# Kernel optimization log

Hardware: AMD Instinct MI355X
Metric: run time of the kernel (lower is better)

## Reference

```python
import jax, jax.numpy as jnp
import numpy as np

B = 48        # graphs
NPG = 64      # nodes per graph
N = B * NPG   # 3072 total nodes
E = B * NPG * NPG  # 196608 fully-connected intra-graph edges
EMB = 8       # ldm latent size
HID = 128     # hidden_size
OUT = 128     # out_size
NL = 3        # n_layers


def setup_inputs() -> dict:
    key = jax.random.key(0)
    ks = jax.random.split(key, 20)
    H = jax.random.normal(ks[0], (N, EMB), jnp.float32)
    Z = jax.random.normal(ks[1], (N, 1, 3), jnp.float32)
    beta = jax.random.uniform(ks[2], (N,), jnp.float32)
    batch_ids = jnp.repeat(jnp.arange(B, dtype=jnp.int32), NPG)
    # variadic_meshgrid: fully-connected edges within each graph
    base = np.arange(B, dtype=np.int32)[:, None, None] * NPG
    r = np.broadcast_to(np.arange(NPG, dtype=np.int32)[:, None], (NPG, NPG))
    row = (base + r[None]).reshape(-1)
    col = (base + r.T[None]).reshape(-1)
    edges = jnp.asarray(np.stack([row, col], axis=0), jnp.int32)

    def lin(k, fan_in, fan_out):
        return jax.random.normal(k, (fan_in, fan_out), jnp.float32) / jnp.sqrt(jnp.float32(fan_in))

    params = {
        'W_emb': lin(ks[3], EMB + 3, HID), 'b_emb': jnp.zeros((HID,), jnp.float32),
        'We1': jnp.stack([lin(jax.random.fold_in(ks[4], l), 2 * HID + 1, HID) for l in range(NL)]),
        'be1': jnp.zeros((NL, HID), jnp.float32),
        'We2': jnp.stack([lin(jax.random.fold_in(ks[5], l), HID, HID) for l in range(NL)]),
        'be2': jnp.zeros((NL, HID), jnp.float32),
        'Wn1': jnp.stack([lin(jax.random.fold_in(ks[6], l), 2 * HID, HID) for l in range(NL)]),
        'bn1': jnp.zeros((NL, HID), jnp.float32),
        'Wn2': jnp.stack([lin(jax.random.fold_in(ks[7], l), HID, HID) for l in range(NL)]),
        'bn2': jnp.zeros((NL, HID), jnp.float32),
        'Wo1': lin(ks[8], HID, HID), 'bo1': jnp.zeros((HID,), jnp.float32),
        'Wo2': lin(ks[9], HID, OUT), 'bo2': jnp.zeros((OUT,), jnp.float32),
    }
    return dict(H=H, Z=Z, beta=beta, batch_ids=batch_ids, edges=edges, **params)


def reference(H, Z, beta, batch_ids, edges, W_emb, b_emb, We1, be1, We2, be2,
              Wn1, bn1, Wn2, bn2, Wo1, bo1, Wo2, bo2):
    # t_embed = [beta, sin(beta), cos(beta)] per node, concatenated to latent H
    t_embed = jnp.stack([beta, jnp.sin(beta), jnp.cos(beta)], axis=-1)  # [N,3]
    h = jnp.concatenate([H, t_embed], axis=-1) @ W_emb + b_emb          # [N,HID]

    row, col = edges[0], edges[1]
    # squared pairwise distance over (channel, xyz)
    d2 = jnp.sum((Z[row] - Z[col]) ** 2, axis=(1, 2))[:, None]          # [E,1]

    # EGNN-style message passing (stand-in for EPT/AMEGNN encoder)
    for l in range(NL):
        m = jax.nn.silu(jnp.concatenate([h[row], h[col], d2], axis=-1) @ We1[l] + be1[l])
        m = jax.nn.silu(m @ We2[l] + be2[l])                            # [E,HID]
        agg = jax.ops.segment_sum(m, row, num_segments=N)               # [N,HID]
        h = h + jax.nn.silu(jnp.concatenate([h, agg], axis=-1) @ Wn1[l] + bn1[l]) @ Wn2[l] + bn2[l]

    # std_conserve_scatter_sum readout: segment-sum / sqrt(count)
    counts = jax.ops.segment_sum(jnp.ones((N,), h.dtype), batch_ids, num_segments=B)
    g = jax.ops.segment_sum(h, batch_ids, num_segments=B) / jnp.sqrt(counts)[:, None]  # [B,HID]

    # linear_out: SiLU -> Linear -> SiLU -> Linear
    out = jax.nn.silu(g) @ Wo1 + bo1
    out = jax.nn.silu(out) @ Wo2 + bo2                                   # [B,OUT]
    return out
```

## Files before the change

kernel.cpp:

```cpp
#include <hip/hip_runtime.h>

#define NGRAPH 48
#define ALPHA 1.44269504088896340736f
#define LN2   0.69314718055994530942f

typedef __bf16 bf16x8 __attribute__((ext_vector_type(8)));
typedef float  f32x16 __attribute__((ext_vector_type(16)));

__device__ __forceinline__ f32x16 MFMA(bf16x8 a, bf16x8 b, f32x16 c) {
  return __builtin_amdgcn_mfma_f32_32x32x16_bf16(a, b, c, 0, 0, 0);
}

__device__ __forceinline__ float fsilu(float x) {
  return x * __builtin_amdgcn_rcpf(1.0f + __expf(-x));
}
__device__ __forceinline__ float ssilu(float s) {
  return s * __builtin_amdgcn_rcpf(1.0f + __builtin_amdgcn_exp2f(-s));
}

__global__ __launch_bounds__(256) void prep_kernel(
    const float* We1, const float* We2, const float* Wn1, const float* Wn2,
    __bf16* We1T, __bf16* We2T, __bf16* Wn1T, __bf16* Wn2T, float* wv) {
  int i = blockIdx.x * 256 + threadIdx.x;
  const int S0 = 3 * 256 * 128;
  const int S1 = 3 * 128 * 128;
  const int S2 = 3 * 128 * 256;
  const int S3 = 3 * 128 * 128;
  const int S4 = 3 * 128;
  if (i < S0) {
    int l = i / (256 * 128); int r = i % (256 * 128); int n = r / 128; int k = r % 128;
    float v = (n < 128) ? We1[(l * 257 + k) * 128 + n]
                        : We1[(l * 257 + 128 + k) * 128 + (n - 128)];
    We1T[i] = (__bf16)v; return;
  }
  i -= S0;
  if (i < S1) {
    int l = i / (128 * 128); int r = i % (128 * 128); int n = r / 128, k = r % 128;
    We2T[i] = (__bf16)We2[(l * 128 + k) * 128 + n]; return;
  }
  i -= S1;
  if (i < S2) {
    int l = i / (128 * 256); int r = i % (128 * 256); int n = r / 256, k = r % 256;
    float sc = (k >= 128) ? LN2 : 1.0f;
    Wn1T[i] = (__bf16)(Wn1[(l * 256 + k) * 128 + n] * sc); return;
  }
  i -= S2;
  if (i < S3) {
    int l = i / (128 * 128); int r = i % (128 * 128); int n = r / 128, k = r % 128;
    Wn2T[i] = (__bf16)Wn2[(l * 128 + k) * 128 + n]; return;
  }
  i -= S3;
  if (i < S4) {
    int l = i / 128, k = i % 128;
    wv[i] = ALPHA * We1[(l * 257 + 256) * 128 + k];
  }
}

__device__ __forceinline__ void pq_stage(const float* hn,
    const __bf16* We1Tl, const float* be1l, float* Pp, __bf16* Qb, int r0, int t) {
  int lane = t & 63, wid = t >> 6;
  int l31 = lane & 31, q = lane >> 5;
  bf16x8 af[8];
#pragma unroll
  for (int kk = 0; kk < 8; ++kk) {
    int k0 = kk * 16 + q * 8;
    const float* ap = &hn[l31 * 132 + k0];
#pragma unroll
    for (int j = 0; j < 8; ++j) af[kk][j] = (__bf16)ap[j];
  }
#pragma unroll
  for (int half = 0; half < 2; ++half) {
    int nt = wid * 2 + half;
    f32x16 acc;
#pragma unroll
    for (int r = 0; r < 16; ++r) acc[r] = 0.f;
#pragma unroll
    for (int kk = 0; kk < 8; ++kk) {
      int k0 = kk * 16 + q * 8;
      bf16x8 b = *(const bf16x8*)&We1Tl[(nt * 32 + l31) * 128 + k0];
      acc = MFMA(af[kk], b, acc);
    }
    int col = nt * 32 + l31;
    if (col < 128) {
      float bb = be1l[col];
#pragma unroll
      for (int reg = 0; reg < 16; ++reg) {
        int rr = (reg & 3) + 8 * (reg >> 2) + 4 * q;
        Pp[(r0 + rr) * 128 + col] = (acc[reg] + bb) * ALPHA;
      }
    } else {
      int c2 = col - 128;
#pragma unroll
      for (int reg = 0; reg < 16; ++reg) {
        int rr = (reg & 3) + 8 * (reg >> 2) + 4 * q;
        Qb[(r0 + rr) * 128 + c2] = (__bf16)(acc[reg] * ALPHA);
      }
    }
  }
}

__global__ __launch_bounds__(256) void embed_kernel(
    const float* H, const float* beta, const float* W_emb, const float* b_emb,
    const __bf16* We1T0, const float* be1_0,
    float* h, float* Pp, __bf16* Qb) {
  __shared__ float Hs[256];
  __shared__ float bet[32], sb[32], cb[32];
  __shared__ float hns[32 * 132];
  int t = threadIdx.x; int r0 = blockIdx.x * 32;
  Hs[t] = H[r0 * 8 + t];
  if (t < 32) {
    float b = beta[r0 + t];
    bet[t] = b; sb[t] = sinf(b); cb[t] = cosf(b);
  }
  __syncthreads();
#pragma unroll
  for (int i = 0; i < 16; ++i) {
    int c = t + 256 * i;
    int row = c >> 7, n = c & 127;
    float acc = b_emb[n];
#pragma unroll
    for (int k = 0; k < 8; ++k) acc += Hs[row * 8 + k] * W_emb[k * 128 + n];
    acc += bet[row] * W_emb[8 * 128 + n] + sb[row] * W_emb[9 * 128 + n]
         + cb[row] * W_emb[10 * 128 + n];
    hns[row * 132 + n] = acc;
    h[(r0 + row) * 128 + n] = acc;
  }
  __syncthreads();
  pq_stage(hns, We1T0, be1_0, Pp, Qb, r0, t);
}

__global__ __launch_bounds__(512)
__attribute__((amdgpu_waves_per_eu(4, 4)))
void edge_kernel(
    const float* __restrict__ Ppin, const __bf16* __restrict__ Qbin,
    const float* __restrict__ Z, const float* __restrict__ wvg,
    const __bf16* __restrict__ We2Tl, const float* __restrict__ be2l,
    float* __restrict__ agg) {
  __shared__ __bf16 Qs[64 * 132];
  __shared__ __bf16 WeTs[128 * 132];
  __shared__ float  Ps[4 * 132];
  __shared__ float  aggp[8][132];
  __shared__ float  Zs[192];
  __shared__ float  wvs[128];
  __shared__ float  be2s[128];
  int t = threadIdx.x;
  int g = blockIdx.x >> 4, atile = blockIdx.x & 15;
  int a0 = atile * 4, gn0 = g * 64;
#pragma unroll
  for (int i = 0; i < 2; ++i) {
    int c = t + 512 * i; int row = c >> 4, c8 = (c & 15) * 8;
    *(uint4*)&Qs[row * 132 + c8] = *(const uint4*)&Qbin[(gn0 + row) * 128 + c8];
  }
#pragma unroll
  for (int i = 0; i < 4; ++i) {
    int c = t + 512 * i; int row = c >> 4, c8 = (c & 15) * 8;
    *(uint4*)&WeTs[row * 132 + c8] = *(const uint4*)&We2Tl[row * 128 + c8];
  }
  if (t < 128) {
    int row = t >> 5, c4 = (t & 31) * 4;
    *(float4*)&Ps[row * 132 + c4] = *(const float4*)&Ppin[(gn0 + a0 + row) * 128 + c4];
    wvs[t] = wvg[t];
    be2s[t] = ALPHA * be2l[t];
  }
  if (t < 192) Zs[t] = Z[gn0 * 3 + t];
  __syncthreads();

  int lane = t & 63, wid = t >> 6, l31 = lane & 31, q = lane >> 5;
  int a_loc = wid >> 1, bhalf = wid & 1;
  int a_g = a0 + a_loc;
  int b = bhalf * 32 + l31;

  float zax = Zs[a_g * 3], zay = Zs[a_g * 3 + 1], zaz = Zs[a_g * 3 + 2];
  float dx = zax - Zs[b * 3], dy = zay - Zs[b * 3 + 1], dz = zaz - Zs[b * 3 + 2];
  float d2 = dx * dx + dy * dy + dz * dz;

  bf16x8 af[8];
#pragma unroll
  for (int kk = 0; kk < 8; ++kk) {
    int k0 = kk * 16 + q * 8;
    float4 pv0 = *(const float4*)&Ps[a_loc * 132 + k0];
    float4 pv1 = *(const float4*)&Ps[a_loc * 132 + k0 + 4];
    float4 wv0 = *(const float4*)&wvs[k0];
    float4 wv1 = *(const float4*)&wvs[k0 + 4];
    bf16x8 qv = *(const bf16x8*)&Qs[b * 132 + k0];
#pragma unroll
    for (int j = 0; j < 4; ++j) {
      af[kk][j]     = (__bf16)ssilu(fmaf(d2, wv0[j], pv0[j]) + (float)qv[j]);
      af[kk][j + 4] = (__bf16)ssilu(fmaf(d2, wv1[j], pv1[j]) + (float)qv[j + 4]);
    }
  }
  float smv[4];
#pragma unroll
  for (int np = 0; np < 2; ++np) {
    f32x16 accA, accB;
#pragma unroll
    for (int r = 0; r < 16; ++r) { accA[r] = 0.f; accB[r] = 0.f; }
#pragma unroll
    for (int kk = 0; kk < 8; ++kk) {
      int ko = kk * 16 + q * 8;
      accA = MFMA(af[kk], *(const bf16x8*)&WeTs[((np * 2 + 0) * 32 + l31) * 132 + ko], accA);
      accB = MFMA(af[kk], *(const bf16x8*)&WeTs[((np * 2 + 1) * 32 + l31) * 132 + ko], accB);
    }
    float bbA = be2s[(np * 2 + 0) * 32 + l31], bbB = be2s[(np * 2 + 1) * 32 + l31];
    float sA0 = 0.f, sA1 = 0.f, sB0 = 0.f, sB1 = 0.f;
#pragma unroll
    for (int r = 0; r < 8; ++r) {
      sA0 += ssilu(accA[r] + bbA); sA1 += ssilu(accA[r + 8] + bbA);
      sB0 += ssilu(accB[r] + bbB); sB1 += ssilu(accB[r + 8] + bbB);
    }
    float sA = sA0 + sA1; sA += __shfl_xor(sA, 32); smv[np * 2 + 0] = sA;
    float sB = sB0 + sB1; sB += __shfl_xor(sB, 32); smv[np * 2 + 1] = sB;
  }
  if (q == 0) {
#pragma unroll
    for (int nt = 0; nt < 4; ++nt)
      aggp[wid][nt * 32 + l31] = smv[nt];
  }
  __syncthreads();
  {
    int row = t >> 7, n = t & 127;
    agg[(gn0 + a0 + row) * 128 + n] = aggp[row * 2 + 0][n] + aggp[row * 2 + 1][n];
  }
}

__global__ __launch_bounds__(256) void node_kernel(
    const float* __restrict__ h, const float* __restrict__ agg,
    const __bf16* __restrict__ Wn1Tl, const float* __restrict__ bn1l,
    const __bf16* __restrict__ Wn2Tl, const float* __restrict__ bn2l,
    const __bf16* __restrict__ We1Tn, const float* __restrict__ be1n,
    float* __restrict__ hout, float* __restrict__ Pp, __bf16* __restrict__ Qb,
    int do_pq) {
  __shared__ float A1s[32 * 260];
  __shared__ float T1s[32 * 132];
  __shared__ float hns[32 * 132];
  int t = threadIdx.x; int r0 = blockIdx.x * 32;
  int lane = t & 63, wid = t >> 6, l31 = lane & 31, q = lane >> 5;
#pragma unroll
  for (int i = 0; i < 8; ++i) {
    int c = t + 256 * i;
    int row = c >> 6, c4 = (c & 63) * 4;
    const float* src = (c4 < 128) ? &h[(r0 + row) * 128 + c4]
                                  : &agg[(r0 + row) * 128 + c4 - 128];
    *(float4*)&A1s[row * 260 + c4] = *(const float4*)src;
  }
  __syncthreads();
  {
    f32x16 acc;
#pragma unroll
    for (int r = 0; r < 16; ++r) acc[r] = 0.f;
#pragma unroll
    for (int kk = 0; kk < 16; ++kk) {
      int k0 = kk * 16 + q * 8;
      bf16x8 a; const float* ap = &A1s[l31 * 260 + k0];
#pragma unroll
      for (int j = 0; j < 8; ++j) a[j] = (__bf16)ap[j];
      bf16x8 b = *(const bf16x8*)&Wn1Tl[(wid * 32 + l31) * 256 + k0];
      acc = MFMA(a, b, acc);
    }
    int col = wid * 32 + l31; float bb = bn1l[col];
#pragma unroll
    for (int reg = 0; reg < 16; ++reg) {
      int rr = (reg & 3) + 8 * (reg >> 2) + 4 * q;
      T1s[rr * 132 + col] = fsilu(acc[reg] + bb);
    }
  }
  __syncthreads();
  {
    f32x16 acc;
#pragma unroll
    for (int r = 0; r < 16; ++r) acc[r] = 0.f;
#pragma unroll
    for (int kk = 0; kk < 8; ++kk) {
      int k0 = kk * 16 + q * 8;
      bf16x8 a; const float* ap = &T1s[l31 * 132 + k0];
#pragma unroll
      for (int j = 0; j < 8; ++j) a[j] = (__bf16)ap[j];
      bf16x8 b = *(const bf16x8*)&Wn2Tl[(wid * 32 + l31) * 128 + k0];
      acc = MFMA(a, b, acc);
    }
    int col = wid * 32 + l31; float bb = bn2l[col];
#pragma unroll
    for (int reg = 0; reg < 16; ++reg) {
      int rr = (reg & 3) + 8 * (reg >> 2) + 4 * q;
      float v = acc[reg] + bb + A1s[rr * 260 + col];
      hns[rr * 132 + col] = v;
      hout[(r0 + rr) * 128 + col] = v;
    }
  }
  __syncthreads();
  if (do_pq) pq_stage(hns, We1Tn, be1n, Pp, Qb, r0, t);
}

__global__ __launch_bounds__(256) void readout_kernel(
    const float* h, const float* Wo1, const float* bo1,
    const float* Wo2, const float* bo2, float* out) {
  __shared__ float part[2][128];
  __shared__ float sbuf[128];
  int g = blockIdx.x; int t = threadIdx.x; int n = t & 127, half = t >> 7;
  float acc = 0.f;
#pragma unroll
  for (int r = 0; r < 32; ++r) acc += h[(g * 64 + half * 32 + r) * 128 + n];
  part[half][n] = acc;
  __syncthreads();
  if (half == 0) sbuf[n] = fsilu((part[0][n] + part[1][n]) * 0.125f);
  __syncthreads();
  float o1 = 0.f;
#pragma unroll
  for (int k = 0; k < 64; ++k) o1 += sbuf[half * 64 + k] * Wo1[(half * 64 + k) * 128 + n];
  part[half][n] = o1;
  __syncthreads();
  if (half == 0) sbuf[n] = fsilu(part[0][n] + part[1][n] + bo1[n]);
  __syncthreads();
  float o2 = 0.f;
#pragma unroll
  for (int k = 0; k < 64; ++k) o2 += sbuf[half * 64 + k] * Wo2[(half * 64 + k) * 128 + n];
  part[half][n] = o2;
  __syncthreads();
  if (half == 0) out[g * 128 + n] = part[0][n] + part[1][n] + bo2[n];
}

extern "C" void kernel_launch(void* const* d_in, const int* in_sizes, int n_in,
                              void* d_out, int out_size, void* d_ws, size_t ws_size,
                              hipStream_t stream) {
  (void)in_sizes; (void)n_in; (void)out_size; (void)ws_size;
  const float* H     = (const float*)d_in[0];
  const float* Z     = (const float*)d_in[1];
  const float* beta  = (const float*)d_in[2];
  const float* W_emb = (const float*)d_in[5];
  const float* b_emb = (const float*)d_in[6];
  const float* We1   = (const float*)d_in[7];
  const float* be1   = (const float*)d_in[8];
  const float* We2   = (const float*)d_in[9];
  const float* be2   = (const float*)d_in[10];
  const float* Wn1   = (const float*)d_in[11];
  const float* bn1   = (const float*)d_in[12];
  const float* Wn2   = (const float*)d_in[13];
  const float* bn2   = (const float*)d_in[14];
  const float* Wo1   = (const float*)d_in[15];
  const float* bo1   = (const float*)d_in[16];
  const float* Wo2   = (const float*)d_in[17];
  const float* bo2   = (const float*)d_in[18];

  char* ws = (char*)d_ws;
  float*  h    = (float*)(ws + 0);
  float*  Pp   = (float*)(ws + 1572864);
  float*  agg  = (float*)(ws + 3145728);
  __bf16* Qb   = (__bf16*)(ws + 4718592);
  __bf16* We1T = (__bf16*)(ws + 5505024);
  __bf16* We2T = (__bf16*)(ws + 5701632);
  __bf16* Wn1T = (__bf16*)(ws + 5799936);
  __bf16* Wn2T = (__bf16*)(ws + 5996544);
  float*  wv   = (float*)(ws + 6094848);

  prep_kernel<<<1154, 256, 0, stream>>>(We1, We2, Wn1, Wn2, We1T, We2T, Wn1T, Wn2T, wv);
  embed_kernel<<<96, 256, 0, stream>>>(H, beta, W_emb, b_emb, We1T, be1, h, Pp, Qb);

  for (int l = 0; l < 3; ++l) {
    edge_kernel<<<NGRAPH * 16, 512, 0, stream>>>(
        Pp, Qb, Z, wv + l * 128, We2T + l * 128 * 128, be2 + l * 128, agg);
    int dopq = (l < 2) ? 1 : 0;
    node_kernel<<<96, 256, 0, stream>>>(
        h, agg, Wn1T + l * 128 * 256, bn1 + l * 128, Wn2T + l * 128 * 128, bn2 + l * 128,
        We1T + (dopq ? (l + 1) * 256 * 128 : 0), be1 + (dopq ? (l + 1) * 128 : 0),
        h, Pp, Qb, dopq);
  }
  readout_kernel<<<NGRAPH, 256, 0, stream>>>(h, Wo1, bo1, Wo2, bo2, (float*)d_out);
}
```

Baseline: 100.8 us.

## Halve edge kernel LDS by staging We2 in two halves, raise occupancy

The edge kernel now keeps only half of the transposed We2 weight tile in shared memory at a time. It reloads the second half after the first two output column tiles are done, and the P tile buffer is reused for the aggregation partials. Lower LDS use and a waves_per_eu hint raised from 4 to 6 aim to fit more blocks per CU. In exchange there are two extra block barriers, a serialized mid-kernel global reload, and tighter register limits that could cause spills given the 8 live bf16x8 A fragments.

```diff
diff --git a/kernel.cpp b/kernel.cpp
--- a/kernel.cpp
+++ b/kernel.cpp
@@ -130,16 +130,15 @@
 }
 
 __global__ __launch_bounds__(512)
-__attribute__((amdgpu_waves_per_eu(4, 4)))
+__attribute__((amdgpu_waves_per_eu(6, 6)))
 void edge_kernel(
     const float* __restrict__ Ppin, const __bf16* __restrict__ Qbin,
     const float* __restrict__ Z, const float* __restrict__ wvg,
     const __bf16* __restrict__ We2Tl, const float* __restrict__ be2l,
     float* __restrict__ agg) {
   __shared__ __bf16 Qs[64 * 132];
-  __shared__ __bf16 WeTs[128 * 132];
-  __shared__ float  Ps[4 * 132];
-  __shared__ float  aggp[8][132];
+  __shared__ __bf16 WeTs[64 * 132];
+  __shared__ float  PsAgg[8 * 132];
   __shared__ float  Zs[192];
   __shared__ float  wvs[128];
   __shared__ float  be2s[128];
@@ -149,16 +148,12 @@
 #pragma unroll
   for (int i = 0; i < 2; ++i) {
     int c = t + 512 * i; int row = c >> 4, c8 = (c & 15) * 8;
-    *(uint4*)&Qs[row * 132 + c8] = *(const uint4*)&Qbin[(gn0 + row) * 128 + c8];
-  }
-#pragma unroll
-  for (int i = 0; i < 4; ++i) {
-    int c = t + 512 * i; int row = c >> 4, c8 = (c & 15) * 8;
+    *(uint4*)&Qs[row * 132 + c8]   = *(const uint4*)&Qbin[(gn0 + row) * 128 + c8];
     *(uint4*)&WeTs[row * 132 + c8] = *(const uint4*)&We2Tl[row * 128 + c8];
   }
   if (t < 128) {
     int row = t >> 5, c4 = (t & 31) * 4;
-    *(float4*)&Ps[row * 132 + c4] = *(const float4*)&Ppin[(gn0 + a0 + row) * 128 + c4];
+    *(float4*)&PsAgg[row * 132 + c4] = *(const float4*)&Ppin[(gn0 + a0 + row) * 128 + c4];
     wvs[t] = wvg[t];
     be2s[t] = ALPHA * be2l[t];
   }
@@ -178,8 +173,8 @@
 #pragma unroll
   for (int kk = 0; kk < 8; ++kk) {
     int k0 = kk * 16 + q * 8;
-    float4 pv0 = *(const float4*)&Ps[a_loc * 132 + k0];
-    float4 pv1 = *(const float4*)&Ps[a_loc * 132 + k0 + 4];
+    float4 pv0 = *(const float4*)&PsAgg[a_loc * 132 + k0];
+    float4 pv1 = *(const float4*)&PsAgg[a_loc * 132 + k0 + 4];
     float4 wv0 = *(const float4*)&wvs[k0];
     float4 wv1 = *(const float4*)&wvs[k0 + 4];
     bf16x8 qv = *(const bf16x8*)&Qs[b * 132 + k0];
@@ -191,35 +186,54 @@
   }
   float smv[4];
 #pragma unroll
-  for (int np = 0; np < 2; ++np) {
-    f32x16 accA, accB;
-#pragma unroll
-    for (int r = 0; r < 16; ++r) { accA[r] = 0.f; accB[r] = 0.f; }
+  for (int nt = 0; nt < 2; ++nt) {
+    f32x16 acc;
+#pragma unroll
+    for (int r = 0; r < 16; ++r) acc[r] = 0.f;
 #pragma unroll
     for (int kk = 0; kk < 8; ++kk) {
       int ko = kk * 16 + q * 8;
-      accA = MFMA(af[kk], *(const bf16x8*)&WeTs[((np * 2 + 0) * 32 + l31) * 132 + ko], accA);
-      accB = MFMA(af[kk], *(const bf16x8*)&WeTs[((np * 2 + 1) * 32 + l31) * 132 + ko], accB);
-    }
-    float bbA = be2s[(np * 2 + 0) * 32 + l31], bbB = be2s[(np * 2 + 1) * 32 + l31];
-    float sA0 = 0.f, sA1 = 0.f, sB0 = 0.f, sB1 = 0.f;
-#pragma unroll
-    for (int r = 0; r < 8; ++r) {
-      sA0 += ssilu(accA[r] + bbA); sA1 += ssilu(accA[r + 8] + bbA);
-      sB0 += ssilu(accB[r] + bbB); sB1 += ssilu(accB[r + 8] + bbB);
-    }
-    float sA = sA0 + sA1; sA += __shfl_xor(sA, 32); smv[np * 2 + 0] = sA;
-    float sB = sB0 + sB1; sB += __shfl_xor(sB, 32); smv[np * 2 + 1] = sB;
+      acc = MFMA(af[kk], *(const bf16x8*)&WeTs[(nt * 32 + l31) * 132 + ko], acc);
+    }
+    float bb = be2s[nt * 32 + l31];
+    float s0 = 0.f, s1 = 0.f;
+#pragma unroll
+    for (int r = 0; r < 8; ++r) { s0 += ssilu(acc[r] + bb); s1 += ssilu(acc[r + 8] + bb); }
+    float s = s0 + s1; s += __shfl_xor(s, 32); smv[nt] = s;
+  }
+  __syncthreads();
+#pragma unroll
+  for (int i = 0; i < 2; ++i) {
+    int c = t + 512 * i; int row = c >> 4, c8 = (c & 15) * 8;
+    *(uint4*)&WeTs[row * 132 + c8] = *(const uint4*)&We2Tl[(64 + row) * 128 + c8];
+  }
+  __syncthreads();
+#pragma unroll
+  for (int nt = 2; nt < 4; ++nt) {
+    f32x16 acc;
+#pragma unroll
+    for (int r = 0; r < 16; ++r) acc[r] = 0.f;
+#pragma unroll
+    for (int kk = 0; kk < 8; ++kk) {
+      int ko = kk * 16 + q * 8;
+      acc = MFMA(af[kk], *(const bf16x8*)&WeTs[((nt - 2) * 32 + l31) * 132 + ko], acc);
+    }
+    float bb = be2s[nt * 32 + l31];
+    float s0 = 0.f, s1 = 0.f;
+#pragma unroll
+    for (int r = 0; r < 8; ++r) { s0 += ssilu(acc[r] + bb); s1 += ssilu(acc[r + 8] + bb); }
+    float s = s0 + s1; s += __shfl_xor(s, 32); smv[nt] = s;
   }
   if (q == 0) {
 #pragma unroll
     for (int nt = 0; nt < 4; ++nt)
-      aggp[wid][nt * 32 + l31] = smv[nt];
+      PsAgg[wid * 132 + nt * 32 + l31] = smv[nt];
   }
   __syncthreads();
   {
     int row = t >> 7, n = t & 127;
-    agg[(gn0 + a0 + row) * 128 + n] = aggp[row * 2 + 0][n] + aggp[row * 2 + 1][n];
+    agg[(gn0 + a0 + row) * 128 + n] =
+        PsAgg[(row * 2 + 0) * 132 + n] + PsAgg[(row * 2 + 1) * 132 + n];
   }
 }
 
```

After: 103.4 us. 2.6% more time.

## Widen edge tiles to 8 sources per block and halve node tile rows

Applied to the files above, without the earlier changes.

The edge kernel now gives each block 8 source nodes, so each wave handles one source against all 64 targets. Every B-fragment load from LDS is reused for two MFMAs, and the cross-wave aggregation through shared memory plus its barrier are gone. Block order is remapped to interleave graphs. The node kernel processes 16 rows per block with zero-padded MFMA inputs to double the block count for parallelism, at the cost of half-empty MFMAs and more register pressure from holding two A-fragment sets.

```diff
diff --git a/kernel.cpp b/kernel.cpp
--- a/kernel.cpp
+++ b/kernel.cpp
@@ -99,6 +99,54 @@
   }
 }
 
+__device__ __forceinline__ void pq_stage16(const float* hn,
+    const __bf16* We1Tl, const float* be1l, float* Pp, __bf16* Qb, int r0, int t) {
+  int lane = t & 63, wid = t >> 6;
+  int l31 = lane & 31, q = lane >> 5;
+  bf16x8 af[8];
+#pragma unroll
+  for (int kk = 0; kk < 8; ++kk) {
+    int k0 = kk * 16 + q * 8;
+    if (l31 < 16) {
+      const float* ap = &hn[l31 * 132 + k0];
+#pragma unroll
+      for (int j = 0; j < 8; ++j) af[kk][j] = (__bf16)ap[j];
+    } else {
+#pragma unroll
+      for (int j = 0; j < 8; ++j) af[kk][j] = (__bf16)0.f;
+    }
+  }
+#pragma unroll
+  for (int half = 0; half < 2; ++half) {
+    int nt = wid * 2 + half;
+    f32x16 acc;
+#pragma unroll
+    for (int r = 0; r < 16; ++r) acc[r] = 0.f;
+#pragma unroll
+    for (int kk = 0; kk < 8; ++kk) {
+      int k0 = kk * 16 + q * 8;
+      bf16x8 b = *(const bf16x8*)&We1Tl[(nt * 32 + l31) * 128 + k0];
+      acc = MFMA(af[kk], b, acc);
+    }
+    int col = nt * 32 + l31;
+    if (col < 128) {
+      float bb = be1l[col];
+#pragma unroll
+      for (int reg = 0; reg < 8; ++reg) {
+        int rr = (reg & 3) + 8 * (reg >> 2) + 4 * q;
+        Pp[(r0 + rr) * 128 + col] = (acc[reg] + bb) * ALPHA;
+      }
+    } else {
+      int c2 = col - 128;
+#pragma unroll
+      for (int reg = 0; reg < 8; ++reg) {
+        int rr = (reg & 3) + 8 * (reg >> 2) + 4 * q;
+        Qb[(r0 + rr) * 128 + c2] = (__bf16)(acc[reg] * ALPHA);
+      }
+    }
+  }
+}
+
 __global__ __launch_bounds__(256) void embed_kernel(
     const float* H, const float* beta, const float* W_emb, const float* b_emb,
     const __bf16* We1T0, const float* be1_0,
@@ -138,14 +186,15 @@
     float* __restrict__ agg) {
   __shared__ __bf16 Qs[64 * 132];
   __shared__ __bf16 WeTs[128 * 132];
-  __shared__ float  Ps[4 * 132];
-  __shared__ float  aggp[8][132];
+  __shared__ float  Ps[8 * 132];
   __shared__ float  Zs[192];
   __shared__ float  wvs[128];
   __shared__ float  be2s[128];
   int t = threadIdx.x;
-  int g = blockIdx.x >> 4, atile = blockIdx.x & 15;
-  int a0 = atile * 4, gn0 = g * 64;
+  int bid = blockIdx.x;
+  int idx = bid >> 3, r8 = bid & 7;
+  int atile = idx & 7, g = (idx >> 3) * 8 + r8;
+  int a0 = atile * 8, gn0 = g * 64;
 #pragma unroll
   for (int i = 0; i < 2; ++i) {
     int c = t + 512 * i; int row = c >> 4, c8 = (c & 15) * 8;
@@ -156,70 +205,68 @@
     int c = t + 512 * i; int row = c >> 4, c8 = (c & 15) * 8;
     *(uint4*)&WeTs[row * 132 + c8] = *(const uint4*)&We2Tl[row * 128 + c8];
   }
-  if (t < 128) {
+  if (t < 256) {
     int row = t >> 5, c4 = (t & 31) * 4;
     *(float4*)&Ps[row * 132 + c4] = *(const float4*)&Ppin[(gn0 + a0 + row) * 128 + c4];
-    wvs[t] = wvg[t];
-    be2s[t] = ALPHA * be2l[t];
+  } else if (t < 384) {
+    int n = t - 256;
+    wvs[n] = wvg[n]; be2s[n] = ALPHA * be2l[n];
   }
   if (t < 192) Zs[t] = Z[gn0 * 3 + t];
   __syncthreads();
 
   int lane = t & 63, wid = t >> 6, l31 = lane & 31, q = lane >> 5;
-  int a_loc = wid >> 1, bhalf = wid & 1;
-  int a_g = a0 + a_loc;
-  int b = bhalf * 32 + l31;
+  int a_loc = wid, a_g = a0 + wid;
 
   float zax = Zs[a_g * 3], zay = Zs[a_g * 3 + 1], zaz = Zs[a_g * 3 + 2];
-  float dx = zax - Zs[b * 3], dy = zay - Zs[b * 3 + 1], dz = zaz - Zs[b * 3 + 2];
-  float d2 = dx * dx + dy * dy + dz * dz;
-
-  bf16x8 af[8];
-#pragma unroll
-  for (int kk = 0; kk < 8; ++kk) {
-    int k0 = kk * 16 + q * 8;
-    float4 pv0 = *(const float4*)&Ps[a_loc * 132 + k0];
-    float4 pv1 = *(const float4*)&Ps[a_loc * 132 + k0 + 4];
-    float4 wv0 = *(const float4*)&wvs[k0];
-    float4 wv1 = *(const float4*)&wvs[k0 + 4];
-    bf16x8 qv = *(const bf16x8*)&Qs[b * 132 + k0];
-#pragma unroll
-    for (int j = 0; j < 4; ++j) {
-      af[kk][j]     = (__bf16)ssilu(fmaf(d2, wv0[j], pv0[j]) + (float)qv[j]);
-      af[kk][j + 4] = (__bf16)ssilu(fmaf(d2, wv1[j], pv1[j]) + (float)qv[j + 4]);
+  bf16x8 af[2][8];
+#pragma unroll
+  for (int bg = 0; bg < 2; ++bg) {
+    int b = bg * 32 + l31;
+    float dx = zax - Zs[b * 3], dy = zay - Zs[b * 3 + 1], dz = zaz - Zs[b * 3 + 2];
+    float d2 = dx * dx + dy * dy + dz * dz;
+#pragma unroll
+    for (int kk = 0; kk < 8; ++kk) {
+      int k0 = kk * 16 + q * 8;
+      float4 pv0 = *(const float4*)&Ps[a_loc * 132 + k0];
+      float4 pv1 = *(const float4*)&Ps[a_loc * 132 + k0 + 4];
+      float4 wv0 = *(const float4*)&wvs[k0];
+      float4 wv1 = *(const float4*)&wvs[k0 + 4];
+      bf16x8 qv = *(const bf16x8*)&Qs[b * 132 + k0];
+#pragma unroll
+      for (int j = 0; j < 4; ++j) {
+        af[bg][kk][j]     = (__bf16)ssilu(fmaf(d2, wv0[j], pv0[j]) + (float)qv[j]);
+        af[bg][kk][j + 4] = (__bf16)ssilu(fmaf(d2, wv1[j], pv1[j]) + (float)qv[j + 4]);
+      }
     }
   }
   float smv[4];
 #pragma unroll
-  for (int np = 0; np < 2; ++np) {
-    f32x16 accA, accB;
-#pragma unroll
-    for (int r = 0; r < 16; ++r) { accA[r] = 0.f; accB[r] = 0.f; }
+  for (int nt = 0; nt < 4; ++nt) {
+    f32x16 acc0, acc1;
+#pragma unroll
+    for (int r = 0; r < 16; ++r) { acc0[r] = 0.f; acc1[r] = 0.f; }
 #pragma unroll
     for (int kk = 0; kk < 8; ++kk) {
-      int ko = kk * 16 + q * 8;
-      accA = MFMA(af[kk], *(const bf16x8*)&WeTs[((np * 2 + 0) * 32 + l31) * 132 + ko], accA);
-      accB = MFMA(af[kk], *(const bf16x8*)&WeTs[((np * 2 + 1) * 32 + l31) * 132 + ko], accB);
-    }
-    float bbA = be2s[(np * 2 + 0) * 32 + l31], bbB = be2s[(np * 2 + 1) * 32 + l31];
-    float sA0 = 0.f, sA1 = 0.f, sB0 = 0.f, sB1 = 0.f;
+      bf16x8 bq = *(const bf16x8*)&WeTs[(nt * 32 + l31) * 132 + kk * 16 + q * 8];
+      acc0 = MFMA(af[0][kk], bq, acc0);
+      acc1 = MFMA(af[1][kk], bq, acc1);
+    }
+    float bb = be2s[nt * 32 + l31];
+    float s0 = 0.f, s1 = 0.f;
 #pragma unroll
     for (int r = 0; r < 8; ++r) {
-      sA0 += ssilu(accA[r] + bbA); sA1 += ssilu(accA[r + 8] + bbA);
-      sB0 += ssilu(accB[r] + bbB); sB1 += ssilu(accB[r + 8] + bbB);
-    }
-    float sA = sA0 + sA1; sA += __shfl_xor(sA, 32); smv[np * 2 + 0] = sA;
-    float sB = sB0 + sB1; sB += __shfl_xor(sB, 32); smv[np * 2 + 1] = sB;
+      s0 += ssilu(acc0[r] + bb) + ssilu(acc1[r] + bb);
+      s1 += ssilu(acc0[r + 8] + bb) + ssilu(acc1[r + 8] + bb);
+    }
+    float s = s0 + s1;
+    s += __shfl_xor(s, 32);
+    smv[nt] = s;
   }
   if (q == 0) {
 #pragma unroll
     for (int nt = 0; nt < 4; ++nt)
-      aggp[wid][nt * 32 + l31] = smv[nt];
-  }
-  __syncthreads();
-  {
-    int row = t >> 7, n = t & 127;
-    agg[(gn0 + a0 + row) * 128 + n] = aggp[row * 2 + 0][n] + aggp[row * 2 + 1][n];
+      agg[(gn0 + a_g) * 128 + nt * 32 + l31] = smv[nt];
   }
 }
 
@@ -230,13 +277,13 @@
     const __bf16* __restrict__ We1Tn, const float* __restrict__ be1n,
     float* __restrict__ hout, float* __restrict__ Pp, __bf16* __restrict__ Qb,
     int do_pq) {
-  __shared__ float A1s[32 * 260];
-  __shared__ float T1s[32 * 132];
-  __shared__ float hns[32 * 132];
-  int t = threadIdx.x; int r0 = blockIdx.x * 32;
+  __shared__ float A1s[16 * 260];
+  __shared__ float T1s[16 * 132];
+  __shared__ float hns[16 * 132];
+  int t = threadIdx.x; int r0 = blockIdx.x * 16;
   int lane = t & 63, wid = t >> 6, l31 = lane & 31, q = lane >> 5;
 #pragma unroll
-  for (int i = 0; i < 8; ++i) {
+  for (int i = 0; i < 4; ++i) {
     int c = t + 256 * i;
     int row = c >> 6, c4 = (c & 63) * 4;
     const float* src = (c4 < 128) ? &h[(r0 + row) * 128 + c4]
@@ -251,15 +298,21 @@
 #pragma unroll
     for (int kk = 0; kk < 16; ++kk) {
       int k0 = kk * 16 + q * 8;
-      bf16x8 a; const float* ap = &A1s[l31 * 260 + k0];
-#pragma unroll
-      for (int j = 0; j < 8; ++j) a[j] = (__bf16)ap[j];
+      bf16x8 a;
+      if (l31 < 16) {
+        const float* ap = &A1s[l31 * 260 + k0];
+#pragma unroll
+        for (int j = 0; j < 8; ++j) a[j] = (__bf16)ap[j];
+      } else {
+#pragma unroll
+        for (int j = 0; j < 8; ++j) a[j] = (__bf16)0.f;
+      }
       bf16x8 b = *(const bf16x8*)&Wn1Tl[(wid * 32 + l31) * 256 + k0];
       acc = MFMA(a, b, acc);
     }
     int col = wid * 32 + l31; float bb = bn1l[col];
 #pragma unroll
-    for (int reg = 0; reg < 16; ++reg) {
+    for (int reg = 0; reg < 8; ++reg) {
       int rr = (reg & 3) + 8 * (reg >> 2) + 4 * q;
       T1s[rr * 132 + col] = fsilu(acc[reg] + bb);
     }
@@ -272,15 +325,21 @@
 #pragma unroll
     for (int kk = 0; kk < 8; ++kk) {
       int k0 = kk * 16 + q * 8;
-      bf16x8 a; const float* ap = &T1s[l31 * 132 + k0];
-#pragma unroll
-      for (int j = 0; j < 8; ++j) a[j] = (__bf16)ap[j];
+      bf16x8 a;
+      if (l31 < 16) {
+        const float* ap = &T1s[l31 * 132 + k0];
+#pragma unroll
+        for (int j = 0; j < 8; ++j) a[j] = (__bf16)ap[j];
+      } else {
+#pragma unroll
+        for (int j = 0; j < 8; ++j) a[j] = (__bf16)0.f;
+      }
       bf16x8 b = *(const bf16x8*)&Wn2Tl[(wid * 32 + l31) * 128 + k0];
       acc = MFMA(a, b, acc);
     }
     int col = wid * 32 + l31; float bb = bn2l[col];
 #pragma unroll
-    for (int reg = 0; reg < 16; ++reg) {
+    for (int reg = 0; reg < 8; ++reg) {
       int rr = (reg & 3) + 8 * (reg >> 2) + 4 * q;
       float v = acc[reg] + bb + A1s[rr * 260 + col];
       hns[rr * 132 + col] = v;
@@ -288,7 +347,7 @@
     }
   }
   __syncthreads();
-  if (do_pq) pq_stage(hns, We1Tn, be1n, Pp, Qb, r0, t);
+  if (do_pq) pq_stage16(hns, We1Tn, be1n, Pp, Qb, r0, t);
 }
 
 __global__ __launch_bounds__(256) void readout_kernel(
@@ -356,10 +415,10 @@
   embed_kernel<<<96, 256, 0, stream>>>(H, beta, W_emb, b_emb, We1T, be1, h, Pp, Qb);
 
   for (int l = 0; l < 3; ++l) {
-    edge_kernel<<<NGRAPH * 16, 512, 0, stream>>>(
+    edge_kernel<<<NGRAPH * 8, 512, 0, stream>>>(
         Pp, Qb, Z, wv + l * 128, We2T + l * 128 * 128, be2 + l * 128, agg);
     int dopq = (l < 2) ? 1 : 0;
-    node_kernel<<<96, 256, 0, stream>>>(
+    node_kernel<<<192, 256, 0, stream>>>(
         h, agg, Wn1T + l * 128 * 256, bn1 + l * 128, Wn2T + l * 128 * 128, bn2 + l * 128,
         We1T + (dopq ? (l + 1) * 256 * 128 : 0), be1 + (dopq ? (l + 1) * 128 : 0),
         h, Pp, Qb, dopq);
```

Result: slower. 151.0 us (+49.8%).

## Raise edge kernel occupancy by cutting registers and LDS, split aggregation buffers

Applied to the files above, without the earlier changes.

The edge kernel now targets 6 waves per EU instead of 4. To fit that, it processes one 32-wide output tile per MFMA loop instead of two, which lowers accumulator register pressure. The shared wv/be2 staging and the final LDS reduction with its extra barrier are removed, and each half-wave group writes its partial sums straight to one of two global buffers. The node kernel adds the two buffers when it loads them. This costs an extra global read in the node kernel, uncached global loads of wv/be2 inside the edge loop, and possible register spills under the tighter waves-per-EU bound.

```diff
diff --git a/kernel.cpp b/kernel.cpp
--- a/kernel.cpp
+++ b/kernel.cpp
@@ -130,19 +130,16 @@
 }
 
 __global__ __launch_bounds__(512)
-__attribute__((amdgpu_waves_per_eu(4, 4)))
+__attribute__((amdgpu_waves_per_eu(6, 6)))
 void edge_kernel(
     const float* __restrict__ Ppin, const __bf16* __restrict__ Qbin,
     const float* __restrict__ Z, const float* __restrict__ wvg,
     const __bf16* __restrict__ We2Tl, const float* __restrict__ be2l,
-    float* __restrict__ agg) {
+    float* __restrict__ agg0, float* __restrict__ agg1) {
   __shared__ __bf16 Qs[64 * 132];
   __shared__ __bf16 WeTs[128 * 132];
   __shared__ float  Ps[4 * 132];
-  __shared__ float  aggp[8][132];
   __shared__ float  Zs[192];
-  __shared__ float  wvs[128];
-  __shared__ float  be2s[128];
   int t = threadIdx.x;
   int g = blockIdx.x >> 4, atile = blockIdx.x & 15;
   int a0 = atile * 4, gn0 = g * 64;
@@ -159,8 +156,6 @@
   if (t < 128) {
     int row = t >> 5, c4 = (t & 31) * 4;
     *(float4*)&Ps[row * 132 + c4] = *(const float4*)&Ppin[(gn0 + a0 + row) * 128 + c4];
-    wvs[t] = wvg[t];
-    be2s[t] = ALPHA * be2l[t];
   }
   if (t < 192) Zs[t] = Z[gn0 * 3 + t];
   __syncthreads();
@@ -180,8 +175,8 @@
     int k0 = kk * 16 + q * 8;
     float4 pv0 = *(const float4*)&Ps[a_loc * 132 + k0];
     float4 pv1 = *(const float4*)&Ps[a_loc * 132 + k0 + 4];
-    float4 wv0 = *(const float4*)&wvs[k0];
-    float4 wv1 = *(const float4*)&wvs[k0 + 4];
+    float4 wv0 = *(const float4*)&wvg[k0];
+    float4 wv1 = *(const float4*)&wvg[k0 + 4];
     bf16x8 qv = *(const bf16x8*)&Qs[b * 132 + k0];
 #pragma unroll
     for (int j = 0; j < 4; ++j) {
@@ -191,40 +186,33 @@
   }
   float smv[4];
 #pragma unroll
-  for (int np = 0; np < 2; ++np) {
-    f32x16 accA, accB;
-#pragma unroll
-    for (int r = 0; r < 16; ++r) { accA[r] = 0.f; accB[r] = 0.f; }
+  for (int nt = 0; nt < 4; ++nt) {
+    f32x16 acc;
+#pragma unroll
+    for (int r = 0; r < 16; ++r) acc[r] = 0.f;
 #pragma unroll
     for (int kk = 0; kk < 8; ++kk) {
       int ko = kk * 16 + q * 8;
-      accA = MFMA(af[kk], *(const bf16x8*)&WeTs[((np * 2 + 0) * 32 + l31) * 132 + ko], accA);
-      accB = MFMA(af[kk], *(const bf16x8*)&WeTs[((np * 2 + 1) * 32 + l31) * 132 + ko], accB);
-    }
-    float bbA = be2s[(np * 2 + 0) * 32 + l31], bbB = be2s[(np * 2 + 1) * 32 + l31];
-    float sA0 = 0.f, sA1 = 0.f, sB0 = 0.f, sB1 = 0.f;
-#pragma unroll
-    for (int r = 0; r < 8; ++r) {
-      sA0 += ssilu(accA[r] + bbA); sA1 += ssilu(accA[r + 8] + bbA);
-      sB0 += ssilu(accB[r] + bbB); sB1 += ssilu(accB[r + 8] + bbB);
-    }
-    float sA = sA0 + sA1; sA += __shfl_xor(sA, 32); smv[np * 2 + 0] = sA;
-    float sB = sB0 + sB1; sB += __shfl_xor(sB, 32); smv[np * 2 + 1] = sB;
+      acc = MFMA(af[kk], *(const bf16x8*)&WeTs[(nt * 32 + l31) * 132 + ko], acc);
+    }
+    float bb = ALPHA * be2l[nt * 32 + l31];
+    float s0 = 0.f, s1 = 0.f;
+#pragma unroll
+    for (int r = 0; r < 8; ++r) { s0 += ssilu(acc[r] + bb); s1 += ssilu(acc[r + 8] + bb); }
+    float s = s0 + s1; s += __shfl_xor(s, 32);
+    smv[nt] = s;
   }
   if (q == 0) {
+    float* ap = bhalf ? agg1 : agg0;
 #pragma unroll
     for (int nt = 0; nt < 4; ++nt)
-      aggp[wid][nt * 32 + l31] = smv[nt];
-  }
-  __syncthreads();
-  {
-    int row = t >> 7, n = t & 127;
-    agg[(gn0 + a0 + row) * 128 + n] = aggp[row * 2 + 0][n] + aggp[row * 2 + 1][n];
+      ap[(gn0 + a_g) * 128 + nt * 32 + l31] = smv[nt];
   }
 }
 
 __global__ __launch_bounds__(256) void node_kernel(
-    const float* __restrict__ h, const float* __restrict__ agg,
+    const float* __restrict__ h,
+    const float* __restrict__ agg0, const float* __restrict__ agg1,
     const __bf16* __restrict__ Wn1Tl, const float* __restrict__ bn1l,
     const __bf16* __restrict__ Wn2Tl, const float* __restrict__ bn2l,
     const __bf16* __restrict__ We1Tn, const float* __restrict__ be1n,
@@ -239,9 +227,14 @@
   for (int i = 0; i < 8; ++i) {
     int c = t + 256 * i;
     int row = c >> 6, c4 = (c & 63) * 4;
-    const float* src = (c4 < 128) ? &h[(r0 + row) * 128 + c4]
-                                  : &agg[(r0 + row) * 128 + c4 - 128];
-    *(float4*)&A1s[row * 260 + c4] = *(const float4*)src;
+    if (c4 < 128) {
+      *(float4*)&A1s[row * 260 + c4] = *(const float4*)&h[(r0 + row) * 128 + c4];
+    } else {
+      float4 x = *(const float4*)&agg0[(r0 + row) * 128 + c4 - 128];
+      float4 y = *(const float4*)&agg1[(r0 + row) * 128 + c4 - 128];
+      x.x += y.x; x.y += y.y; x.z += y.z; x.w += y.w;
+      *(float4*)&A1s[row * 260 + c4] = x;
+    }
   }
   __syncthreads();
   {
@@ -344,23 +337,25 @@
   char* ws = (char*)d_ws;
   float*  h    = (float*)(ws + 0);
   float*  Pp   = (float*)(ws + 1572864);
-  float*  agg  = (float*)(ws + 3145728);
-  __bf16* Qb   = (__bf16*)(ws + 4718592);
-  __bf16* We1T = (__bf16*)(ws + 5505024);
-  __bf16* We2T = (__bf16*)(ws + 5701632);
-  __bf16* Wn1T = (__bf16*)(ws + 5799936);
-  __bf16* Wn2T = (__bf16*)(ws + 5996544);
-  float*  wv   = (float*)(ws + 6094848);
+  float*  agg0 = (float*)(ws + 3145728);
+  float*  agg1 = (float*)(ws + 4718592);
+  __bf16* Qb   = (__bf16*)(ws + 6291456);
+  __bf16* We1T = (__bf16*)(ws + 7077888);
+  __bf16* We2T = (__bf16*)(ws + 7274496);
+  __bf16* Wn1T = (__bf16*)(ws + 7372800);
+  __bf16* Wn2T = (__bf16*)(ws + 7569408);
+  float*  wv   = (float*)(ws + 7667712);
 
   prep_kernel<<<1154, 256, 0, stream>>>(We1, We2, Wn1, Wn2, We1T, We2T, Wn1T, Wn2T, wv);
   embed_kernel<<<96, 256, 0, stream>>>(H, beta, W_emb, b_emb, We1T, be1, h, Pp, Qb);
 
   for (int l = 0; l < 3; ++l) {
     edge_kernel<<<NGRAPH * 16, 512, 0, stream>>>(
-        Pp, Qb, Z, wv + l * 128, We2T + l * 128 * 128, be2 + l * 128, agg);
+        Pp, Qb, Z, wv + l * 128, We2T + l * 128 * 128, be2 + l * 128, agg0, agg1);
     int dopq = (l < 2) ? 1 : 0;
     node_kernel<<<96, 256, 0, stream>>>(
-        h, agg, Wn1T + l * 128 * 256, bn1 + l * 128, Wn2T + l * 128 * 128, bn2 + l * 128,
+        h, agg0, agg1,
+        Wn1T + l * 128 * 256, bn1 + l * 128, Wn2T + l * 128 * 128, bn2 + l * 128,
         We1T + (dopq ? (l + 1) * 256 * 128 : 0), be1 + (dopq ? (l + 1) * 128 : 0),
         h, Pp, Qb, dopq);
   }
```

Measured after the change: 109.5 us. +8.6%, slower.
